# Performance work log

Hardware: AMD Instinct MI355X
Metric: run time of the kernel (lower is better)

Reference implementation:

```python
import jax, jax.numpy as jnp
import numpy as np


def setup_inputs() -> dict:
    key = jax.random.key(0)
    k1, k2 = jax.random.split(key)
    B, N, M, D = 8, 2048, 2048, 1024
    x = jax.random.normal(k1, (B, N, D), dtype=jnp.float32)
    y = jax.random.normal(k2, (B, M, D), dtype=jnp.float32)
    return {"x": x, "y": y}


def reference(x, y):
    # scores: [B, N, M] = x @ y^T
    scores = jnp.einsum("bnd,bmd->bnm", x, y)
    # row-normalized attention over M (axis=2 of scores)
    attn_row = jax.nn.softmax(scores, axis=2)
    # column-normalized attention: softmax over N of scores^T, i.e. axis=1 then transpose
    attn_col = jax.nn.softmax(scores, axis=1)  # [B, N, M], normalized over N
    A = jnp.einsum("bnm,bmd->bnd", attn_row, y)          # attended summary of y per x-token
    Bout = jnp.einsum("bnm,bnd->bmd", attn_col, x)       # attended summary of x per y-token
    return (A, Bout)
```

## Files before the change

### kernel.cpp

```cpp
#include <hip/hip_runtime.h>
#include <cstdint>
#include <cstddef>

namespace {

constexpr int Bb = 8;
constexpr int Nn = 2048;
constexpr int Dd = 1024;
constexpr int NT = 64;

typedef _Float16 half8 __attribute__((ext_vector_type(8)));
typedef float f32x2v __attribute__((ext_vector_type(2)));
typedef float f32x4v __attribute__((ext_vector_type(4)));
typedef float f32x16v __attribute__((ext_vector_type(16)));
typedef unsigned int v2u __attribute__((ext_vector_type(2)));
typedef unsigned int v4u __attribute__((ext_vector_type(4)));

__device__ __forceinline__ float fast_exp2(float x) {
  float r;
  asm("v_exp_f32 %0, %1\n\ts_nop 1" : "=v"(r) : "v"(x));
  return r;
}

__device__ __forceinline__ unsigned cvt2(float a, float b) {
  return __builtin_bit_cast(unsigned, __builtin_amdgcn_cvt_pkrtz(a, b));
}

template <int CTRL>
__device__ __forceinline__ float dpp_f(float v) {
  return __builtin_bit_cast(
      float, __builtin_amdgcn_update_dpp(0, __builtin_bit_cast(int, v), CTRL,
                                         0xF, 0xF, true));
}
__device__ __forceinline__ float red16_max(float v) {
  v = fmaxf(v, dpp_f<0xB1>(v));
  v = fmaxf(v, dpp_f<0x4E>(v));
  v = fmaxf(v, dpp_f<0x124>(v));
  v = fmaxf(v, dpp_f<0x128>(v));
  return v;
}
__device__ __forceinline__ float red16_add(float v) {
  v = v + dpp_f<0xB1>(v);
  v = v + dpp_f<0x4E>(v);
  v = v + dpp_f<0x124>(v);
  v = v + dpp_f<0x128>(v);
  return v;
}

__device__ __forceinline__ void barrier_lgkm() {
  asm volatile("s_waitcnt lgkmcnt(0)" ::: "memory");
  __builtin_amdgcn_s_barrier();
  __builtin_amdgcn_sched_barrier(0);
}
__device__ __forceinline__ void barrier_lgkm15() {
  asm volatile("s_waitcnt lgkmcnt(15)" ::: "memory");
  __builtin_amdgcn_s_barrier();
  __builtin_amdgcn_sched_barrier(0);
}

__global__ void convf16(const float* __restrict__ in, v4u* __restrict__ out) {
  const int n8 = Bb * Nn * Dd / 8;
  int i = blockIdx.x * blockDim.x + threadIdx.x;
  const int stride = gridDim.x * blockDim.x;
  const f32x4v* in4 = (const f32x4v*)in;
  for (; i < n8; i += stride) {
    f32x4v a = in4[2 * i], b = in4[2 * i + 1];
    v4u p;
    p[0] = cvt2(a[0], a[1]);
    p[1] = cvt2(a[2], a[3]);
    p[2] = cvt2(b[0], b[1]);
    p[3] = cvt2(b[2], b[3]);
    out[i] = p;
  }
}

template <int WS>
__device__ __forceinline__ v4u ld8h(const float* f32p, const v4u* h16p) {
  if constexpr (WS) {
    return *h16p;
  } else {
    f32x4v a = *(const f32x4v*)f32p;
    f32x4v b = *(const f32x4v*)(f32p + 4);
    v4u p;
    p[0] = cvt2(a[0], a[1]);
    p[1] = cvt2(a[2], a[3]);
    p[2] = cvt2(b[0], b[1]);
    p[3] = cvt2(b[2], b[3]);
    return p;
  }
}

template <int WS>
__global__ __launch_bounds__(512, 2) void flash_fwd(
    const float* __restrict__ Qf, const float* __restrict__ Yf,
    const v4u* __restrict__ Qw, const v4u* __restrict__ Yw,
    float* __restrict__ Om) {
  __shared__ __attribute__((aligned(128))) char ybuf[2][65536];
  __shared__ __attribute__((aligned(16))) float pscr2[4][32][36];
  __shared__ __attribute__((aligned(16))) char Pb[2048];
  __shared__ float sscale[32];
  __shared__ float sinvl[32];
  __shared__ int flags[2];

  const int tid = (int)threadIdx.x;
  const int w = tid >> 6, l = tid & 63;
  const int lm = l & 15, g = (l >> 4) & 3, g2 = (l >> 5) & 1, l31 = l & 31;
  const int kvf = w >> 2, ds = w & 3;
  const int bid = (int)blockIdx.x, batch = bid & 7, row0 = (bid >> 3) * 32;
  const size_t bY = (size_t)batch * Nn;

  v4u qreg[2][8];
#pragma unroll
  for (int qh = 0; qh < 2; ++qh)
#pragma unroll
    for (int ks = 0; ks < 8; ++ks) {
      const int rr = row0 + qh * 16 + lm;
      const int dd_ = ds * 256 + ks * 32 + g * 8;
      qreg[qh][ks] = ld8h<WS>(Qf + (size_t)(bY + rr) * Dd + dd_,
                              Qw + (size_t)(bY + rr) * 128 + (dd_ >> 3));
    }

#define LOADY(dst, t_)                                                        \
  do {                                                                        \
    const int rr_ = (t_)*32 + kvf * 16 + lm;                                  \
    _Pragma("unroll") for (int ks = 0; ks < 8; ++ks) {                        \
      const int dd_ = ds * 256 + ks * 32 + g * 8;                             \
      dst[ks] = ld8h<WS>(Yf + (size_t)(bY + rr_) * Dd + dd_,                  \
                         Yw + (size_t)(bY + rr_) * 128 + (dd_ >> 3));         \
    }                                                                         \
  } while (0)

  const unsigned sbase =
      (unsigned)((kvf * 4 + (lm >> 2)) * 8192 + (ds * 16 + (g >> 1)) * 128 +
                 (lm & 3) * 32 + (g & 1) * 16);
#define STAGE_WR(SRC, BASE)                                                   \
  do {                                                                        \
    _Pragma("unroll") for (int ks = 0; ks < 8; ++ks)                          \
        *(v4u*)((BASE) + sbase + ks * 256) = SRC[ks];                         \
  } while (0)

  char* const yb0 = &ybuf[0][0];
  v4u s[8];
  LOADY(s, 0);
  STAGE_WR(s, yb0);
  if (tid == 0) {
    flags[0] = 0;
    flags[1] = 0;
  }

  f32x16v Oacc[4];
#pragma unroll
  for (int i = 0; i < 4; ++i)
#pragma unroll
    for (int j = 0; j < 16; ++j) Oacc[i][j] = 0.0f;

  float m_run = -__builtin_inff();
  float l_run = 0.0f;
  const unsigned ylds = (unsigned)(uintptr_t)yb0;
  constexpr float L2E = 1.44269504088896f;

  __syncthreads();

  for (int t = 0; t < NT; ++t) {
    const unsigned ytr = ylds + (unsigned)((t & 1) * 65536);
    char* const ybn = yb0 + (((t + 1) & 1) * 65536);

    f32x4v acc0 = {0.f, 0.f, 0.f, 0.f}, acc1 = {0.f, 0.f, 0.f, 0.f};
#pragma unroll
    for (int ks = 0; ks < 8; ++ks) {
      half8 av = __builtin_bit_cast(half8, s[ks]);
      acc0 = __builtin_amdgcn_mfma_f32_16x16x32_f16(
          av, __builtin_bit_cast(half8, qreg[0][ks]), acc0, 0, 0, 0);
      acc1 = __builtin_amdgcn_mfma_f32_16x16x32_f16(
          av, __builtin_bit_cast(half8, qreg[1][ks]), acc1, 0, 0, 0);
    }
    LOADY(s, (t + 1) & 63);
    *(f32x4v*)&pscr2[ds][lm][kvf * 16 + g * 4] = acc0;
    *(f32x4v*)&pscr2[ds][16 + lm][kvf * 16 + g * 4] = acc1;
    barrier_lgkm();

    {
      const int rq = 4 * w + (l >> 4);
      const int c = l & 15;
      float s0 = 0.f, s1 = 0.f;
#pragma unroll
      for (int sl = 0; sl < 4; ++sl) {
        f32x2v p_ = *(const f32x2v*)&pscr2[sl][rq][2 * c];
        s0 += p_[0];
        s1 += p_[1];
      }
      float pm = red16_max(fmaxf(s0, s1));
      bool defer = (pm <= m_run + 8.0f);
      bool allw = (bool)__all((int)defer);
      float scale = 1.0f;
      if (!allw) {
        float mn = fmaxf(m_run, pm);
        scale = fast_exp2((m_run - mn) * L2E);
        m_run = mn;
      }
      float e0 = fast_exp2((s0 - m_run) * L2E);
      float e1 = fast_exp2((s1 - m_run) * L2E);
      float ps = red16_add(e0 + e1);
      l_run = l_run * scale + ps;
      *(unsigned*)(Pb + (c >> 2) * 512 + rq * 16 + (c & 3) * 4) = cvt2(e0, e1);
      if (c == 0) sscale[rq] = scale;
      if (l == 0 && !allw) flags[t & 1] = 1;
    }
    if (tid == 0) flags[(t + 1) & 1] = 0;

    v2u trr[16];
#pragma unroll
    for (int kb = 0; kb < 2; ++kb)
#pragma unroll
      for (int df = 0; df < 4; ++df) {
        const unsigned wb =
            ytr + (unsigned)((kb * 4 + g2 * 2) * 8192 +
                             ((w * 4 + df) * 2 + (l31 >> 4)) * 128 +
                             (l31 & 15) * 8);
        asm volatile("ds_read_b64_tr_b16 %0, %1"
                     : "=v"(trr[kb * 8 + df * 2])
                     : "v"(wb));
        asm volatile("ds_read_b64_tr_b16 %0, %1"
                     : "=v"(trr[kb * 8 + df * 2 + 1])
                     : "v"(wb + 8192u));
      }
    STAGE_WR(s, ybn);
    barrier_lgkm15();

    const int flg = flags[t & 1];
    half8 pa0 = *(const half8*)(Pb + g2 * 512 + l31 * 16);
    half8 pa1 = *(const half8*)(Pb + (2 + g2) * 512 + l31 * 16);
    if (flg) {
#pragma unroll
      for (int df = 0; df < 4; ++df)
#pragma unroll
        for (int r = 0; r < 16; ++r) {
          const int q_ = (r & 3) + 8 * (r >> 2) + 4 * g2;
          Oacc[df][r] *= sscale[q_];
        }
    }
    asm volatile("s_waitcnt lgkmcnt(0)" ::: "memory");
    __builtin_amdgcn_sched_barrier(0);
#pragma unroll
    for (int kb = 0; kb < 2; ++kb)
#pragma unroll
      for (int df = 0; df < 4; ++df) {
        v4u bu;
        bu[0] = trr[kb * 8 + df * 2][0];
        bu[1] = trr[kb * 8 + df * 2][1];
        bu[2] = trr[kb * 8 + df * 2 + 1][0];
        bu[3] = trr[kb * 8 + df * 2 + 1][1];
        Oacc[df] = __builtin_amdgcn_mfma_f32_32x32x16_f16(
            kb ? pa1 : pa0, __builtin_bit_cast(half8, bu), Oacc[df], 0, 0, 0);
      }
  }

  if ((l & 15) == 0) sinvl[4 * w + (l >> 4)] = 1.0f / l_run;
  __syncthreads();
#pragma unroll
  for (int df = 0; df < 4; ++df)
#pragma unroll
    for (int r = 0; r < 16; ++r) {
      const int q_ = (r & 3) + 8 * (r >> 2) + 4 * g2;
      const float inv = sinvl[q_];
      Om[(size_t)(bY + row0 + q_) * Dd + (w * 4 + df) * 32 + l31] =
          Oacc[df][r] * inv;
    }
#undef STAGE_WR
#undef LOADY
}

}

extern "C" void kernel_launch(void* const* d_in, const int* in_sizes, int n_in,
                              void* d_out, int out_size, void* d_ws,
                              size_t ws_size, hipStream_t stream) {
  (void)in_sizes; (void)n_in; (void)out_size;
  const float* x = (const float*)d_in[0];
  const float* y = (const float*)d_in[1];
  float* A = (float*)d_out;
  float* Bo = A + (size_t)Bb * Nn * Dd;
  const size_t halfws = (size_t)Bb * Nn * Dd * 2;
  dim3 fg(512), fb(512);
  if (d_ws != nullptr && ws_size >= 2 * halfws) {
    v4u* Xw = (v4u*)d_ws;
    v4u* Yw = (v4u*)((char*)d_ws + halfws);
    hipLaunchKernelGGL(convf16, dim3(2048), dim3(256), 0, stream, x, Xw);
    hipLaunchKernelGGL(convf16, dim3(2048), dim3(256), 0, stream, y, Yw);
    hipLaunchKernelGGL(flash_fwd<1>, fg, fb, 0, stream, x, y, Xw, Yw, A);
    hipLaunchKernelGGL(flash_fwd<1>, fg, fb, 0, stream, y, x, Yw, Xw, Bo);
  } else {
    hipLaunchKernelGGL(flash_fwd<0>, fg, fb, 0, stream, x, y, (const v4u*)x,
                       (const v4u*)y, A);
    hipLaunchKernelGGL(flash_fwd<0>, fg, fb, 0, stream, y, x, (const v4u*)y,
                       (const v4u*)x, Bo);
  }
}
```

Measured before the change: 661.1 us.

## Stage Y tiles via direct global-to-LDS DMA loads instead of register staging

When the fp16 workspace is available, the Y tile for the next step is copied straight from global memory into LDS with global_load_lds, with no pass through registers and no ds_write. The QK MFMA operands are then read from LDS instead of registers, and the score accumulation is split into two independent chains per row block to shorten MFMA dependency chains. The rescale flag becomes a per-wave flag array that is OR-reduced, which drops the separate flag reset. The changes free VGPRs and LDS-write work but add an extra barrier per iteration and a full vmcnt wait at the end of each step.

After: 633.1 us. 1.04x faster.

```diff
diff --git a/kernel.cpp b/kernel.cpp
--- a/kernel.cpp
+++ b/kernel.cpp
@@ -52,8 +52,7 @@
   __builtin_amdgcn_s_barrier();
   __builtin_amdgcn_sched_barrier(0);
 }
-__device__ __forceinline__ void barrier_lgkm15() {
-  asm volatile("s_waitcnt lgkmcnt(15)" ::: "memory");
+__device__ __forceinline__ void barrier_plain() {
   __builtin_amdgcn_s_barrier();
   __builtin_amdgcn_sched_barrier(0);
 }
@@ -100,7 +99,7 @@
   __shared__ __attribute__((aligned(16))) char Pb[2048];
   __shared__ float sscale[32];
   __shared__ float sinvl[32];
-  __shared__ int flags[2];
+  __shared__ __attribute__((aligned(16))) int sflag8[8];
 
   const int tid = (int)threadIdx.x;
   const int w = tid >> 6, l = tid & 63;
@@ -119,6 +118,23 @@
       qreg[qh][ks] = ld8h<WS>(Qf + (size_t)(bY + rr) * Dd + dd_,
                               Qw + (size_t)(bY + rr) * 128 + (dd_ >> 3));
     }
+
+  const unsigned sbase =
+      (unsigned)((kvf * 4 + (lm >> 2)) * 8192 + (ds * 16 + (g >> 1)) * 128 +
+                 (lm & 3) * 32 + (g & 1) * 16);
+
+#define DMA_STAGE(t_, SLOT)                                                   \
+  do {                                                                        \
+    const int rl_ = (t_)*32 + (w << 2) + ((l >> 1) & 3);                      \
+    const v4u* gp_ = Yw + (size_t)(bY + rl_) * 128 + ((l >> 3) << 1) + (l & 1); \
+    char* lp_ = &ybuf[(SLOT)][0] + w * 8192;                                  \
+    _Pragma("unroll") for (int j = 0; j < 8; ++j) {                           \
+      __builtin_amdgcn_global_load_lds(                                       \
+          (const __attribute__((address_space(1))) unsigned*)(const void*)(gp_ + j * 16), \
+          (__attribute__((address_space(3))) unsigned*)(void*)(lp_ + j * 1024), \
+          16, 0, 0);                                                          \
+    }                                                                         \
+  } while (0)
 
 #define LOADY(dst, t_)                                                        \
   do {                                                                        \
@@ -129,23 +145,20 @@
                          Yw + (size_t)(bY + rr_) * 128 + (dd_ >> 3));         \
     }                                                                         \
   } while (0)
-
-  const unsigned sbase =
-      (unsigned)((kvf * 4 + (lm >> 2)) * 8192 + (ds * 16 + (g >> 1)) * 128 +
-                 (lm & 3) * 32 + (g & 1) * 16);
 #define STAGE_WR(SRC, BASE)                                                   \
   do {                                                                        \
     _Pragma("unroll") for (int ks = 0; ks < 8; ++ks)                          \
         *(v4u*)((BASE) + sbase + ks * 256) = SRC[ks];                         \
   } while (0)
 
-  char* const yb0 = &ybuf[0][0];
   v4u s[8];
-  LOADY(s, 0);
-  STAGE_WR(s, yb0);
-  if (tid == 0) {
-    flags[0] = 0;
-    flags[1] = 0;
+  if constexpr (WS) {
+    DMA_STAGE(0, 0);
+    asm volatile("s_waitcnt vmcnt(0)" ::: "memory");
+  } else {
+    LOADY(s, 0);
+    STAGE_WR(s, &ybuf[0][0]);
+    LOADY(s, 1);
   }
 
   f32x16v Oacc[4];
@@ -156,25 +169,58 @@
 
   float m_run = -__builtin_inff();
   float l_run = 0.0f;
-  const unsigned ylds = (unsigned)(uintptr_t)yb0;
+  const unsigned ylds = (unsigned)(uintptr_t)&ybuf[0][0];
   constexpr float L2E = 1.44269504088896f;
 
+  v2u trr[16];
+
+#define ISSUE_TR(TRBASE)                                                      \
+  do {                                                                        \
+    _Pragma("unroll") for (int kb = 0; kb < 2; ++kb)                          \
+        _Pragma("unroll") for (int df = 0; df < 4; ++df) {                    \
+      const unsigned wb =                                                     \
+          (TRBASE) + (unsigned)((kb * 4 + g2 * 2) * 8192 +                    \
+                                ((w * 4 + df) * 2 + (l31 >> 4)) * 128 +       \
+                                (l31 & 15) * 8);                              \
+      asm volatile("ds_read_b64_tr_b16 %0, %1"                                \
+                   : "=v"(trr[kb * 8 + df * 2])                               \
+                   : "v"(wb));                                                \
+      asm volatile("ds_read_b64_tr_b16 %0, %1"                                \
+                   : "=v"(trr[kb * 8 + df * 2 + 1])                           \
+                   : "v"(wb + 8192u));                                        \
+    }                                                                         \
+  } while (0)
+
   __syncthreads();
 
   for (int t = 0; t < NT; ++t) {
+    const char* ybc = &ybuf[t & 1][0];
     const unsigned ytr = ylds + (unsigned)((t & 1) * 65536);
-    char* const ybn = yb0 + (((t + 1) & 1) * 65536);
-
-    f32x4v acc0 = {0.f, 0.f, 0.f, 0.f}, acc1 = {0.f, 0.f, 0.f, 0.f};
+
+    if constexpr (WS) DMA_STAGE((t + 1) & 63, (t + 1) & 1);
+    f32x4v a0a = {0.f, 0.f, 0.f, 0.f}, a0b = {0.f, 0.f, 0.f, 0.f};
+    f32x4v a1a = {0.f, 0.f, 0.f, 0.f}, a1b = {0.f, 0.f, 0.f, 0.f};
 #pragma unroll
     for (int ks = 0; ks < 8; ++ks) {
-      half8 av = __builtin_bit_cast(half8, s[ks]);
-      acc0 = __builtin_amdgcn_mfma_f32_16x16x32_f16(
-          av, __builtin_bit_cast(half8, qreg[0][ks]), acc0, 0, 0, 0);
-      acc1 = __builtin_amdgcn_mfma_f32_16x16x32_f16(
-          av, __builtin_bit_cast(half8, qreg[1][ks]), acc1, 0, 0, 0);
-    }
-    LOADY(s, (t + 1) & 63);
+      half8 av;
+      if constexpr (WS) {
+        av = *(const half8*)(ybc + sbase + ks * 256);
+      } else {
+        av = __builtin_bit_cast(half8, s[ks]);
+      }
+      if (ks < 4) {
+        a0a = __builtin_amdgcn_mfma_f32_16x16x32_f16(
+            av, __builtin_bit_cast(half8, qreg[0][ks]), a0a, 0, 0, 0);
+        a1a = __builtin_amdgcn_mfma_f32_16x16x32_f16(
+            av, __builtin_bit_cast(half8, qreg[1][ks]), a1a, 0, 0, 0);
+      } else {
+        a0b = __builtin_amdgcn_mfma_f32_16x16x32_f16(
+            av, __builtin_bit_cast(half8, qreg[0][ks]), a0b, 0, 0, 0);
+        a1b = __builtin_amdgcn_mfma_f32_16x16x32_f16(
+            av, __builtin_bit_cast(half8, qreg[1][ks]), a1b, 0, 0, 0);
+      }
+    }
+    f32x4v acc0 = a0a + a0b, acc1 = a1a + a1b;
     *(f32x4v*)&pscr2[ds][lm][kvf * 16 + g * 4] = acc0;
     *(f32x4v*)&pscr2[ds][16 + lm][kvf * 16 + g * 4] = acc1;
     barrier_lgkm();
@@ -204,33 +250,16 @@
       l_run = l_run * scale + ps;
       *(unsigned*)(Pb + (c >> 2) * 512 + rq * 16 + (c & 3) * 4) = cvt2(e0, e1);
       if (c == 0) sscale[rq] = scale;
-      if (l == 0 && !allw) flags[t & 1] = 1;
-    }
-    if (tid == 0) flags[(t + 1) & 1] = 0;
-
-    v2u trr[16];
-#pragma unroll
-    for (int kb = 0; kb < 2; ++kb)
-#pragma unroll
-      for (int df = 0; df < 4; ++df) {
-        const unsigned wb =
-            ytr + (unsigned)((kb * 4 + g2 * 2) * 8192 +
-                             ((w * 4 + df) * 2 + (l31 >> 4)) * 128 +
-                             (l31 & 15) * 8);
-        asm volatile("ds_read_b64_tr_b16 %0, %1"
-                     : "=v"(trr[kb * 8 + df * 2])
-                     : "v"(wb));
-        asm volatile("ds_read_b64_tr_b16 %0, %1"
-                     : "=v"(trr[kb * 8 + df * 2 + 1])
-                     : "v"(wb + 8192u));
-      }
-    STAGE_WR(s, ybn);
-    barrier_lgkm15();
-
-    const int flg = flags[t & 1];
+      if (l == 0) sflag8[w] = allw ? 0 : 1;
+    }
+    ISSUE_TR(ytr);
+    barrier_lgkm();
+
     half8 pa0 = *(const half8*)(Pb + g2 * 512 + l31 * 16);
     half8 pa1 = *(const half8*)(Pb + (2 + g2) * 512 + l31 * 16);
-    if (flg) {
+    v4u f0 = *(const v4u*)&sflag8[0];
+    v4u f1 = *(const v4u*)&sflag8[4];
+    if (f0[0] | f0[1] | f0[2] | f0[3] | f1[0] | f1[1] | f1[2] | f1[3]) {
 #pragma unroll
       for (int df = 0; df < 4; ++df)
 #pragma unroll
@@ -253,6 +282,15 @@
         Oacc[df] = __builtin_amdgcn_mfma_f32_32x32x16_f16(
             kb ? pa1 : pa0, __builtin_bit_cast(half8, bu), Oacc[df], 0, 0, 0);
       }
+
+    if constexpr (WS) {
+      asm volatile("s_waitcnt vmcnt(0)" ::: "memory");
+      barrier_plain();
+    } else {
+      STAGE_WR(s, &ybuf[(t + 1) & 1][0]);
+      LOADY(s, (t + 2) & 63);
+      barrier_lgkm();
+    }
   }
 
   if ((l & 15) == 0) sinvl[4 * w + (l >> 4)] = 1.0f / l_run;
@@ -266,8 +304,10 @@
       Om[(size_t)(bY + row0 + q_) * Dd + (w * 4 + df) * 32 + l31] =
           Oacc[df][r] * inv;
     }
+#undef ISSUE_TR
 #undef STAGE_WR
 #undef LOADY
+#undef DMA_STAGE
 }
 
 }
```
